# Kernel optimization log

Hardware: AMD Instinct MI355X
Metric: run time of the kernel (lower is better)

## Reference

```python
import jax, jax.numpy as jnp
import numpy as np

NUM_EXPERTS = 64
TOP_K = 2
NOISE_STD = 1.0
LOAD_BALANCE_WEIGHT = 0.01
NOISE_KEY = jax.random.fold_in(jax.random.key(0), 12345)


def setup_inputs() -> dict:
    key = jax.random.key(0)
    k1, k2, k3 = jax.random.split(key, 3)
    B, S, D = 4, 4096, 1024
    x = jax.random.normal(k1, (B, S, D), dtype=jnp.float32)
    W_gate = jax.random.normal(k2, (NUM_EXPERTS, D), dtype=jnp.float32) * (1.0 / np.sqrt(D))
    W_noise = jax.random.normal(k3, (NUM_EXPERTS, D), dtype=jnp.float32) * (1.0 / np.sqrt(D))
    return {"x": x, "W_gate": W_gate, "W_noise": W_noise}


def reference(x, W_gate, W_noise):
    # x: [B,S,D], W_gate/W_noise: [E,D] (torch Linear weight layout)
    clean_logits = jnp.einsum("bsd,ed->bse", x, W_gate)           # [B,S,E]
    noise_scale = jax.nn.softplus(jnp.einsum("bsd,ed->bse", x, W_noise))
    noise = jax.random.normal(NOISE_KEY, clean_logits.shape, clean_logits.dtype)
    logits = clean_logits + noise * noise_scale * NOISE_STD

    probs = jax.nn.softmax(logits, axis=-1)                        # [B,S,E]
    routing_weights, expert_indices = jax.lax.top_k(probs, TOP_K)  # [B,S,K]
    routing_weights = routing_weights / jnp.sum(routing_weights, axis=-1, keepdims=True)

    # Load-balance loss on clean logits
    B, S, E = clean_logits.shape
    num_tokens = B * S
    expert_mask = jax.nn.one_hot(expert_indices, E, dtype=jnp.float32).sum(axis=2)  # [B,S,E]
    tokens_per_expert = expert_mask.sum(axis=(0, 1))               # [E]
    fraction_tokens = tokens_per_expert / num_tokens
    router_probs = jax.nn.softmax(clean_logits, axis=-1)
    mean_router_prob = router_probs.mean(axis=(0, 1))              # [E]
    load_balance_loss = LOAD_BALANCE_WEIGHT * E * jnp.sum(fraction_tokens * mean_router_prob)

    noise_scale_mean = noise_scale.mean()
    return (routing_weights, expert_indices, load_balance_loss, router_probs, noise_scale_mean)
```

## Files before the change

kernel.cpp:

```cpp
#include <hip/hip_runtime.h>
#include <stdint.h>

#define TOKENS 16384
#define DDIM   1024
#define NEXP   64
#define NCOL   128
#define TB     64
#define NBLK   (TOKENS / TB)
#define NCH    (DDIM / 32)
#define NTILE  8
#define CPP    4

typedef __attribute__((ext_vector_type(8))) short bf16x8;
typedef __attribute__((ext_vector_type(4))) float f32x4;

__device__ ushort g_wf[3][NTILE][NCH][64][8];
__device__ float g_ps[NEXP];
__device__ float g_cnt[NEXP];
__device__ float g_spa[1];

__device__ inline ushort bf16rne(float f) {
  uint32_t u = __float_as_uint(f);
  return (ushort)((u + 0x7fffu + ((u >> 16) & 1u)) >> 16);
}
__device__ inline float bf16tof(ushort h) {
  return __uint_as_float(((uint32_t)h) << 16);
}
__device__ inline void split3(float v, ushort& h, ushort& m, ushort& l) {
  h = bf16rne(v);
  float r1 = v - bf16tof(h);
  m = bf16rne(r1);
  float r2 = r1 - bf16tof(m);
  l = bf16rne(r2);
}

struct U2 { uint32_t a, b; };

__host__ __device__ constexpr U2 tf2x32(uint32_t k0, uint32_t k1,
                                        uint32_t x0, uint32_t x1) {
  uint32_t ks[3] = {k0, k1, k0 ^ k1 ^ 0x1BD11BDAu};
  const uint32_t rot[2][4] = {{13u, 15u, 26u, 6u}, {17u, 29u, 16u, 24u}};
  x0 += ks[0]; x1 += ks[1];
  for (int d = 0; d < 5; ++d) {
    for (int j = 0; j < 4; ++j) {
      uint32_t r = rot[d & 1][j];
      x0 += x1;
      x1 = (x1 << r) | (x1 >> (32u - r));
      x1 ^= x0;
    }
    x0 += ks[(d + 1) % 3];
    x1 += ks[(d + 2) % 3] + (uint32_t)(d + 1);
  }
  return U2{x0, x1};
}

__device__ inline uint32_t noise_bits(uint32_t i) {
  constexpr U2 NK = tf2x32(0u, 0u, 0u, 12345u);
  U2 o = tf2x32(NK.a, NK.b, 0u, i);
  return o.a ^ o.b;
}

__device__ inline float xla_erfinv(float x) {
  float w = -log1pf(-x * x);
  float p;
  if (w < 5.0f) {
    w = w - 2.5f;
    p = 2.81022636e-08f;
    p = 3.43273939e-07f + p * w;
    p = -3.5233877e-06f + p * w;
    p = -4.39150654e-06f + p * w;
    p = 0.00021858087f + p * w;
    p = -0.00125372503f + p * w;
    p = -0.00417768164f + p * w;
    p = 0.246640727f + p * w;
    p = 1.50140941f + p * w;
  } else {
    w = sqrtf(w) - 3.0f;
    p = -0.000200214257f;
    p = 0.000100950558f + p * w;
    p = 0.00134934322f + p * w;
    p = -0.00367342844f + p * w;
    p = 0.00573950773f + p * w;
    p = -0.0076224613f + p * w;
    p = 0.00943887047f + p * w;
    p = 1.00167406f + p * w;
    p = 2.83297682f + p * w;
  }
  return p * x;
}

__device__ inline float noise_normal(uint32_t i) {
  uint32_t bits = noise_bits(i);
  float f = __uint_as_float((bits >> 9) | 0x3f800000u) - 1.0f;
  float u = f * 2.0f + (-0.99999994f);
  u = fmaxf(u, -0.99999994f);
  return 1.41421356237f * xla_erfinv(u);
}

__device__ inline float softplus_ref(float x) {
  return fmaxf(x, 0.0f) + log1pf(expf(-fabsf(x)));
}

__device__ inline float wave_max64(float v) {
  #pragma unroll
  for (int off = 32; off; off >>= 1) v = fmaxf(v, __shfl_xor(v, off, 64));
  return v;
}
__device__ inline float wave_sum64(float v) {
  #pragma unroll
  for (int off = 32; off; off >>= 1) v += __shfl_xor(v, off, 64);
  return v;
}
__device__ inline void wave_argmax64(float v, int idx, float& mv, int& mi) {
  float bv = v; int bi = idx;
  #pragma unroll
  for (int off = 32; off; off >>= 1) {
    float ov = __shfl_xor(bv, off, 64);
    int   oi = __shfl_xor(bi, off, 64);
    if (ov > bv || (ov == bv && oi < bi)) { bv = ov; bi = oi; }
  }
  mv = bv; mi = bi;
}

__global__ __launch_bounds__(64)
void wsplit_kernel(const float* __restrict__ wg, const float* __restrict__ wn) {
  const int ct   = blockIdx.x >> 5;
  const int kc   = blockIdx.x & 31;
  const int lane = threadIdx.x;
  const int col  = ct * 16 + (lane & 15);
  const int koff = kc * 32 + (lane >> 4) * 8;
  const float* src = (col < NEXP) ? (wg + (size_t)col * DDIM)
                                  : (wn + (size_t)(col - NEXP) * DDIM);
  const float4 v0 = *(const float4*)&src[koff];
  const float4 v1 = *(const float4*)&src[koff + 4];
  const float av[8] = {v0.x, v0.y, v0.z, v0.w, v1.x, v1.y, v1.z, v1.w};
  union BF8 { bf16x8 v; ushort u[8]; };
  BF8 H, M, L;
  #pragma unroll
  for (int j = 0; j < 8; ++j) {
    ushort h, m, l;
    split3(av[j], h, m, l);
    H.u[j] = h; M.u[j] = m; L.u[j] = l;
  }
  *(bf16x8*)&g_wf[0][ct][kc][lane][0] = H.v;
  *(bf16x8*)&g_wf[1][ct][kc][lane][0] = M.v;
  *(bf16x8*)&g_wf[2][ct][kc][lane][0] = L.v;

  if (blockIdx.x == 0) {
    g_ps[lane] = 0.0f; g_cnt[lane] = 0.0f;
    if (lane == 0) g_spa[0] = 0.0f;
  }
}

#define PHASE_BARRIER()                                      \
  asm volatile("s_waitcnt lgkmcnt(0)" ::: "memory");         \
  __builtin_amdgcn_s_barrier();                              \
  asm volatile("" ::: "memory");

__global__ __launch_bounds__(1024, 4)
void NoisyTopKRouter_57621281243491_kernel(
    const float* __restrict__ x, float* __restrict__ out) {
  __shared__ ushort ldsA[3][4][CPP][64][8];

  const int tid  = threadIdx.x;
  const int w    = tid >> 6;
  const int lane = tid & 63;
  const int ct   = w >> 1;
  const int tgp  = w & 1;
  const int tok0 = blockIdx.x * TB;

  char* LA = (char*)&ldsA[0][0][0][0][0];

  const int srow = tid >> 4;
  const int skq  = tid & 15;
  const int stg  = srow >> 4;
  const int sfr  = srow & 15;
  const int sc   = skq >> 2;
  const int ss   = skq & 3;
  const int so   = (sc * 1024 + ss * 256 + sfr * 16) ^ ((skq & 15) << 4);
  const float* sx = x + (size_t)(tok0 + srow) * DDIM + skq * 8;

  const int fr_row = lane & 15;
  const int fr_s   = lane >> 4;
  const ushort* wf = &g_wf[0][0][0][0][0];
  const int b0 = ct * 16384 + lane * 8;
  #define PS 131072
  const int abA = (tgp * 2) * 4096;
  const int abB = abA + 4096;

  f32x4 accA = {0.f, 0.f, 0.f, 0.f};
  f32x4 accB = {0.f, 0.f, 0.f, 0.f};

  float4 xa0, xa1, xb0, xb1;

  #define SPLIT_PHASE(X0, X1)                                             \
    {                                                                     \
      union BF8 { bf16x8 v; ushort u[8]; };                               \
      BF8 H, M, L;                                                        \
      const float av_[8] = {X0.x, X0.y, X0.z, X0.w, X1.x, X1.y, X1.z, X1.w}; \
      _Pragma("unroll")                                                   \
      for (int j = 0; j < 8; ++j) {                                       \
        ushort h_, m_, l_;                                                \
        split3(av_[j], h_, m_, l_);                                       \
        H.u[j] = h_; M.u[j] = m_; L.u[j] = l_;                            \
      }                                                                   \
      *(bf16x8*)(LA + stg * 4096 + so)         = H.v;                     \
      *(bf16x8*)(LA + 16384 + stg * 4096 + so) = M.v;                     \
      *(bf16x8*)(LA + 32768 + stg * 4096 + so) = L.v;                     \
    }

  #define MFMA_PHASE(ph)                                                  \
    __builtin_amdgcn_s_setprio(1);                                        \
    _Pragma("unroll")                                                     \
    for (int c = 0; c < CPP; ++c) {                                       \
      int ro = c * 1024 + lane * 16;                                      \
      ro ^= ((ro >> 8) & 15) << 4;                                        \
      const bf16x8 AhA = *(const bf16x8*)(LA + abA + ro);                 \
      const bf16x8 AmA = *(const bf16x8*)(LA + 16384 + abA + ro);         \
      const bf16x8 AlA = *(const bf16x8*)(LA + 32768 + abA + ro);         \
      const bf16x8 AhB = *(const bf16x8*)(LA + abB + ro);                 \
      const bf16x8 AmB = *(const bf16x8*)(LA + 16384 + abB + ro);         \
      const bf16x8 AlB = *(const bf16x8*)(LA + 32768 + abB + ro);         \
      const int co = ((ph) * CPP + c) * 512;                              \
      const bf16x8 Bh = *(const bf16x8*)&wf[b0 + co];                     \
      const bf16x8 Bm = *(const bf16x8*)&wf[b0 + PS + co];                \
      const bf16x8 Bl = *(const bf16x8*)&wf[b0 + 2 * PS + co];            \
      accA = __builtin_amdgcn_mfma_f32_16x16x32_bf16(AhA, Bh, accA, 0, 0, 0); \
      accA = __builtin_amdgcn_mfma_f32_16x16x32_bf16(AhA, Bm, accA, 0, 0, 0); \
      accA = __builtin_amdgcn_mfma_f32_16x16x32_bf16(AmA, Bh, accA, 0, 0, 0); \
      accA = __builtin_amdgcn_mfma_f32_16x16x32_bf16(AhA, Bl, accA, 0, 0, 0); \
      accA = __builtin_amdgcn_mfma_f32_16x16x32_bf16(AlA, Bh, accA, 0, 0, 0); \
      accA = __builtin_amdgcn_mfma_f32_16x16x32_bf16(AmA, Bm, accA, 0, 0, 0); \
      accB = __builtin_amdgcn_mfma_f32_16x16x32_bf16(AhB, Bh, accB, 0, 0, 0); \
      accB = __builtin_amdgcn_mfma_f32_16x16x32_bf16(AhB, Bm, accB, 0, 0, 0); \
      accB = __builtin_amdgcn_mfma_f32_16x16x32_bf16(AmB, Bh, accB, 0, 0, 0); \
      accB = __builtin_amdgcn_mfma_f32_16x16x32_bf16(AhB, Bl, accB, 0, 0, 0); \
      accB = __builtin_amdgcn_mfma_f32_16x16x32_bf16(AlB, Bh, accB, 0, 0, 0); \
      accB = __builtin_amdgcn_mfma_f32_16x16x32_bf16(AmB, Bm, accB, 0, 0, 0); \
    }                                                                     \
    __builtin_amdgcn_s_setprio(0);

  #define DO_PHASE(ph, C0, C1, N0, N1, PRE)                               \
    SPLIT_PHASE(C0, C1);                                                  \
    if (PRE) {                                                            \
      N0 = *(const float4*)&sx[(ph + 1) * 128];                           \
      N1 = *(const float4*)&sx[(ph + 1) * 128 + 4];                       \
    }                                                                     \
    PHASE_BARRIER();                                                      \
    MFMA_PHASE(ph);                                                       \
    PHASE_BARRIER();

  xa0 = *(const float4*)&sx[0];
  xa1 = *(const float4*)&sx[4];

  DO_PHASE(0, xa0, xa1, xb0, xb1, 1);
  DO_PHASE(1, xb0, xb1, xa0, xa1, 1);
  DO_PHASE(2, xa0, xa1, xb0, xb1, 1);
  DO_PHASE(3, xb0, xb1, xa0, xa1, 1);
  DO_PHASE(4, xa0, xa1, xb0, xb1, 1);
  DO_PHASE(5, xb0, xb1, xa0, xa1, 1);
  DO_PHASE(6, xa0, xa1, xb0, xb1, 1);
  DO_PHASE(7, xb0, xb1, xa0, xa1, 0);

  #undef DO_PHASE
  #undef SPLIT_PHASE
  #undef MFMA_PHASE
  #undef PS

  float (*lds_logits)[NCOL + 4] = (float (*)[NCOL + 4])LA;
  float (*lps)[NEXP] = (float (*)[NEXP])(LA + 33792);
  float (*lcb)[NEXP] = (float (*)[NEXP])(LA + 37888);
  float* lspw        = (float*)(LA + 41984);

  #pragma unroll
  for (int r = 0; r < 4; ++r) {
    lds_logits[(tgp * 2) * 16 + 4 * fr_s + r][ct * 16 + fr_row]     = accA[r];
    lds_logits[(tgp * 2 + 1) * 16 + 4 * fr_s + r][ct * 16 + fr_row] = accB[r];
  }
  __syncthreads();

  float* out_rw  = out;
  float* out_idx = out + 2 * TOKENS;
  float* out_rp  = out + 4 * TOKENS + 1;

  float ps_acc = 0.0f, sp_acc = 0.0f, c_acc = 0.0f;

  for (int it = 0; it < 4; ++it) {
    const int tl = w * 4 + it;
    const int t  = tok0 + tl;
    const float cl = lds_logits[tl][lane];
    const float nl = lds_logits[tl][NEXP + lane];

    const float m  = wave_max64(cl);
    const float v  = expf(cl - m);
    const float Z  = wave_sum64(v);
    const float rp = v / Z;
    out_rp[(size_t)t * NEXP + lane] = rp;
    ps_acc += rp;

    const float ns  = softplus_ref(nl);
    sp_acc += ns;
    const float noi = noise_normal((uint32_t)(t * NEXP + lane));
    const float lgn = __fadd_rn(cl, __fmul_rn(noi, ns));

    const float m2 = wave_max64(lgn);
    const float v2 = expf(lgn - m2);
    const float Z2 = wave_sum64(v2);
    const float p  = v2 / Z2;

    float p1; int i1;
    wave_argmax64(p, lane, p1, i1);
    const float pm = (lane == i1) ? -3.402823466e38f : p;
    float p2; int i2;
    wave_argmax64(pm, lane, p2, i2);

    c_acc += (float)((lane == i1) + (lane == i2));

    if (lane == 0) {
      const float s = p1 + p2;
      out_rw[t * 2 + 0]  = p1 / s;
      out_rw[t * 2 + 1]  = p2 / s;
      out_idx[t * 2 + 0] = (float)i1;
      out_idx[t * 2 + 1] = (float)i2;
    }
  }

  lps[w][lane] = ps_acc;
  lcb[w][lane] = c_acc;
  const float spw = wave_sum64(sp_acc);
  if (lane == 0) lspw[w] = spw;
  __syncthreads();
  if (tid < NEXP) {
    float a = 0.0f, b = 0.0f;
    #pragma unroll
    for (int j = 0; j < 16; ++j) { a += lps[j][tid]; b += lcb[j][tid]; }
    atomicAdd(&g_ps[tid],  a);
    atomicAdd(&g_cnt[tid], b);
  }
  if (tid == 0) {
    float s = 0.0f;
    #pragma unroll
    for (int j = 0; j < 16; ++j) s += lspw[j];
    atomicAdd(&g_spa[0], s);
  }
}

__global__ void finalize_kernel(float* __restrict__ out) {
  const int lane = threadIdx.x;
  float term = (g_cnt[lane] / (float)TOKENS) * (g_ps[lane] / (float)TOKENS);
  #pragma unroll
  for (int off = 32; off; off >>= 1) term += __shfl_xor(term, off, 64);
  if (lane == 0) {
    out[4 * TOKENS] = 0.64f * term;
    out[4 * TOKENS + 1 + TOKENS * NEXP] = g_spa[0] / (float)(TOKENS * NEXP);
  }
}

extern "C" void kernel_launch(void* const* d_in, const int* in_sizes, int n_in,
                              void* d_out, int out_size, void* d_ws, size_t ws_size,
                              hipStream_t stream) {
  const float* x  = (const float*)d_in[0];
  const float* wg = (const float*)d_in[1];
  const float* wn = (const float*)d_in[2];
  float* out = (float*)d_out;

  (void)d_ws; (void)ws_size; (void)in_sizes; (void)n_in; (void)out_size;

  wsplit_kernel<<<NTILE * NCH, 64, 0, stream>>>(wg, wn);
  NoisyTopKRouter_57621281243491_kernel<<<NBLK, 1024, 0, stream>>>(x, out);
  finalize_kernel<<<1, 64, 0, stream>>>(out);
}
```

Baseline: 138.3 us.

## Double-buffer LDS A tiles to overlap split with MFMA and drop a barrier

Doubles the shared-memory A buffer so the bf16 split of the next K-phase is written into the alternate buffer while MFMAs consume the current one. This removes one of the two block-wide barriers per phase and lets the conversion ALU work overlap the matrix work. The cost is twice the LDS footprint (96KB per block), which may reduce occupancy, and the prefetch now runs one phase further ahead.

```diff
diff --git a/kernel.cpp b/kernel.cpp
--- a/kernel.cpp
+++ b/kernel.cpp
@@ -160,7 +160,7 @@
 __global__ __launch_bounds__(1024, 4)
 void NoisyTopKRouter_57621281243491_kernel(
     const float* __restrict__ x, float* __restrict__ out) {
-  __shared__ ushort ldsA[3][4][CPP][64][8];
+  __shared__ ushort ldsA[2][3][4][CPP][64][8];
 
   const int tid  = threadIdx.x;
   const int w    = tid >> 6;
@@ -169,7 +169,8 @@
   const int tgp  = w & 1;
   const int tok0 = blockIdx.x * TB;
 
-  char* LA = (char*)&ldsA[0][0][0][0][0];
+  char* LA = (char*)&ldsA[0][0][0][0][0][0];
+  #define BUFSZ 49152
 
   const int srow = tid >> 4;
   const int skq  = tid & 15;
@@ -193,7 +194,7 @@
 
   float4 xa0, xa1, xb0, xb1;
 
-  #define SPLIT_PHASE(X0, X1)                                             \
+  #define SPLIT_PHASE(BUF, X0, X1)                                        \
     {                                                                     \
       union BF8 { bf16x8 v; ushort u[8]; };                               \
       BF8 H, M, L;                                                        \
@@ -204,23 +205,24 @@
         split3(av_[j], h_, m_, l_);                                       \
         H.u[j] = h_; M.u[j] = m_; L.u[j] = l_;                            \
       }                                                                   \
-      *(bf16x8*)(LA + stg * 4096 + so)         = H.v;                     \
-      *(bf16x8*)(LA + 16384 + stg * 4096 + so) = M.v;                     \
-      *(bf16x8*)(LA + 32768 + stg * 4096 + so) = L.v;                     \
+      *(bf16x8*)(LA + (BUF) * BUFSZ + stg * 4096 + so)         = H.v;     \
+      *(bf16x8*)(LA + (BUF) * BUFSZ + 16384 + stg * 4096 + so) = M.v;     \
+      *(bf16x8*)(LA + (BUF) * BUFSZ + 32768 + stg * 4096 + so) = L.v;     \
     }
 
-  #define MFMA_PHASE(ph)                                                  \
+  #define MFMA_PHASE(ph, BUF)                                             \
     __builtin_amdgcn_s_setprio(1);                                        \
     _Pragma("unroll")                                                     \
     for (int c = 0; c < CPP; ++c) {                                       \
       int ro = c * 1024 + lane * 16;                                      \
       ro ^= ((ro >> 8) & 15) << 4;                                        \
-      const bf16x8 AhA = *(const bf16x8*)(LA + abA + ro);                 \
-      const bf16x8 AmA = *(const bf16x8*)(LA + 16384 + abA + ro);         \
-      const bf16x8 AlA = *(const bf16x8*)(LA + 32768 + abA + ro);         \
-      const bf16x8 AhB = *(const bf16x8*)(LA + abB + ro);                 \
-      const bf16x8 AmB = *(const bf16x8*)(LA + 16384 + abB + ro);         \
-      const bf16x8 AlB = *(const bf16x8*)(LA + 32768 + abB + ro);         \
+      const char* BB = LA + (BUF) * BUFSZ;                                \
+      const bf16x8 AhA = *(const bf16x8*)(BB + abA + ro);                 \
+      const bf16x8 AmA = *(const bf16x8*)(BB + 16384 + abA + ro);         \
+      const bf16x8 AlA = *(const bf16x8*)(BB + 32768 + abA + ro);         \
+      const bf16x8 AhB = *(const bf16x8*)(BB + abB + ro);                 \
+      const bf16x8 AmB = *(const bf16x8*)(BB + 16384 + abB + ro);         \
+      const bf16x8 AlB = *(const bf16x8*)(BB + 32768 + abB + ro);         \
       const int co = ((ph) * CPP + c) * 512;                              \
       const bf16x8 Bh = *(const bf16x8*)&wf[b0 + co];                     \
       const bf16x8 Bm = *(const bf16x8*)&wf[b0 + PS + co];                \
@@ -240,29 +242,33 @@
     }                                                                     \
     __builtin_amdgcn_s_setprio(0);
 
-  #define DO_PHASE(ph, C0, C1, N0, N1, PRE)                               \
-    SPLIT_PHASE(C0, C1);                                                  \
+  #define DO_REGION(ph, C0, C1, N0, N1, PRE)                              \
+    SPLIT_PHASE((ph + 1) & 1, C0, C1);                                    \
     if (PRE) {                                                            \
-      N0 = *(const float4*)&sx[(ph + 1) * 128];                           \
-      N1 = *(const float4*)&sx[(ph + 1) * 128 + 4];                       \
+      N0 = *(const float4*)&sx[(ph + 2) * 128];                           \
+      N1 = *(const float4*)&sx[(ph + 2) * 128 + 4];                       \
     }                                                                     \
-    PHASE_BARRIER();                                                      \
-    MFMA_PHASE(ph);                                                       \
+    MFMA_PHASE(ph, (ph) & 1);                                             \
     PHASE_BARRIER();
 
   xa0 = *(const float4*)&sx[0];
   xa1 = *(const float4*)&sx[4];
-
-  DO_PHASE(0, xa0, xa1, xb0, xb1, 1);
-  DO_PHASE(1, xb0, xb1, xa0, xa1, 1);
-  DO_PHASE(2, xa0, xa1, xb0, xb1, 1);
-  DO_PHASE(3, xb0, xb1, xa0, xa1, 1);
-  DO_PHASE(4, xa0, xa1, xb0, xb1, 1);
-  DO_PHASE(5, xb0, xb1, xa0, xa1, 1);
-  DO_PHASE(6, xa0, xa1, xb0, xb1, 1);
-  DO_PHASE(7, xb0, xb1, xa0, xa1, 0);
-
-  #undef DO_PHASE
+  SPLIT_PHASE(0, xa0, xa1);
+  xb0 = *(const float4*)&sx[128];
+  xb1 = *(const float4*)&sx[132];
+  PHASE_BARRIER();
+
+  DO_REGION(0, xb0, xb1, xa0, xa1, 1);
+  DO_REGION(1, xa0, xa1, xb0, xb1, 1);
+  DO_REGION(2, xb0, xb1, xa0, xa1, 1);
+  DO_REGION(3, xa0, xa1, xb0, xb1, 1);
+  DO_REGION(4, xb0, xb1, xa0, xa1, 1);
+  DO_REGION(5, xa0, xa1, xb0, xb1, 1);
+  DO_REGION(6, xb0, xb1, xa0, xa1, 0);
+  MFMA_PHASE(7, 1);
+  PHASE_BARRIER();
+
+  #undef DO_REGION
   #undef SPLIT_PHASE
   #undef MFMA_PHASE
   #undef PS
@@ -343,6 +349,7 @@
     for (int j = 0; j < 16; ++j) s += lspw[j];
     atomicAdd(&g_spa[0], s);
   }
+  #undef BUFSZ
 }
 
 __global__ void finalize_kernel(float* __restrict__ out) {
```

After: 139.1 us. No clear change (+0.5%).
